# Optimization experiments

Hardware: AMD Instinct MI355X
Metric: run time of the kernel (lower is better)

## Reference

```python
import jax, jax.numpy as jnp
import numpy as np
import math

DIM = 512
HEADS = 8
B = 16
P = 2048
REL_MAX = 64
REL_SIZE = 2 * REL_MAX + 1
RANK = 4
ALPHA = 16.0
QBITS = 4


def simq(w, bits=QBITS):
    # symmetric linear fake-quantization (matches simulate_quantization)
    qmin = -2 ** (bits - 1)
    qmax = 2 ** (bits - 1) - 1
    m = jnp.max(jnp.abs(w))
    scale = m / qmax
    q = jnp.clip(jnp.round(w / (scale + 1e-8)), qmin, qmax) * scale
    return jnp.where(m == 0, w, q)


def lora_lin(x, W, b, A, LB):
    # F.linear with quantized weight/bias + LoRA path
    out = x @ simq(W).T + simq(b)
    return out + (x @ A.T @ LB.T) * (ALPHA / RANK)


def setup_inputs() -> dict:
    key = jax.random.key(0)
    ks = jax.random.split(key, 20)
    d2 = DIM * 2
    inp = {
        "curr_pos": 2048,
        "z_curr_ri": jax.random.normal(ks[0], (B, DIM, 2), jnp.float32),
        "z_past_ri": jax.random.normal(ks[1], (P, B, DIM, 2), jnp.float32),
        "rel_bias_ri": jax.random.normal(ks[2], (REL_SIZE, DIM, 2), jnp.float32) * 0.02,
    }
    names = ["q", "k", "v", "o"]
    for i, n in enumerate(names):
        kw, ka, kb = jax.random.split(ks[3 + i], 3)
        inp["W" + n] = jax.random.normal(kw, (d2, d2), jnp.float32) / math.sqrt(d2)
        inp["b" + n] = jnp.zeros((d2,), jnp.float32)
        inp["A" + n] = jax.random.normal(ka, (RANK, d2), jnp.float32) / math.sqrt(d2)
        inp["LB" + n] = jax.random.normal(kb, (d2, RANK), jnp.float32) * 0.01
    return inp


def reference(curr_pos, z_curr_ri, z_past_ri, rel_bias_ri,
              Wq, bq, Aq, LBq, Wk, bk, Ak, LBk,
              Wv, bv, Av, LBv, Wo, bo, Ao, LBo):
    Bsz = z_curr_ri.shape[0]
    past_len = z_past_ri.shape[0]
    dim = z_curr_ri.shape[1]
    hd = dim // HEADS

    # projections on real-view of complex inputs ([.., dim, 2] -> [.., 2*dim])
    q = lora_lin(z_curr_ri.reshape(Bsz, dim * 2), Wq, bq, Aq, LBq)
    k = lora_lin(z_past_ri.reshape(past_len, Bsz, dim * 2), Wk, bk, Ak, LBk)
    v = lora_lin(z_past_ri.reshape(past_len, Bsz, dim * 2), Wv, bv, Av, LBv)

    q = q.reshape(Bsz, HEADS, hd, 2)            # [B,H,hd,2]
    k = k.reshape(past_len, Bsz, HEADS, hd, 2)  # [P,B,H,hd,2]
    v = v.reshape(past_len, Bsz, HEADS, hd, 2)
    qr, qi = q[..., 0], q[..., 1]
    kr, ki = k[..., 0], k[..., 1]
    vr, vi = v[..., 0], v[..., 1]

    # Re(q * conj(k)) summed over head_dim -> [B,H,P]
    dot = jnp.einsum('bhd,pbhd->bhp', qr, kr) + jnp.einsum('bhd,pbhd->bhp', qi, ki)

    # relative positional bias lookup (clamped index)
    rel_d = jnp.arange(curr_pos - past_len, curr_pos)
    idx = jnp.clip(rel_d + REL_MAX, 0, rel_bias_ri.shape[0] - 1)
    rb = rel_bias_ri[idx].reshape(past_len, HEADS, hd, 2)  # [P,H,hd,2]
    rel = jnp.einsum('bhd,phd->bhp', qr, rb[..., 0]) + jnp.einsum('bhd,phd->bhp', qi, rb[..., 1])

    w = jax.nn.softmax((dot + rel) / math.sqrt(hd), axis=-1)  # [B,H,P]

    # real softmax weights applied to complex values
    out_r = jnp.einsum('bhp,pbhd->bhd', w, vr)
    out_i = jnp.einsum('bhp,pbhd->bhd', w, vi)
    out_ri = jnp.stack([out_r, out_i], axis=-1).reshape(Bsz, dim * 2)

    o = lora_lin(out_ri, Wo, bo, Ao, LBo)
    return o.reshape(Bsz, dim, 2)  # real view of complex output [B,dim]
```

## Files before the change

### kernel.cpp

```cpp
#include <hip/hip_runtime.h>
#include <math.h>

typedef _Float16 f16;
typedef _Float16 f16x8 __attribute__((ext_vector_type(8)));
typedef _Float16 f16x4 __attribute__((ext_vector_type(4)));
typedef float f32x4 __attribute__((ext_vector_type(4)));

#define NP 2048
#define M_ROWS 32768

#define OFF_ABSMAX 0u
#define OFF_TQ     256u
#define OFF_TO     512u
#define OFF_QBIAS  1024u
#define OFF_XQH    32768u
#define OFF_XQL    65536u
#define OFF_XOH    98304u
#define OFF_XOL    131072u
#define OFF_QBUF   163840u
#define OFF_ATT    229376u
#define OFF_PM     294912u
#define OFF_PL     299008u
#define OFF_PO     303104u
#define OFF_WH     1048576u
#define OFF_TK     9437184u
#define OFF_TV     9961472u
#define OFF_KV     10485760u

__device__ __forceinline__ float qint_of(float w, float scale) {
    return fminf(7.f, fmaxf(-8.f, rintf(w / (scale + 1e-8f))));
}

__device__ __forceinline__ void gload16(const void* g, void* l) {
  __builtin_amdgcn_global_load_lds((const __attribute__((address_space(1))) void*)g,
                                   (__attribute__((address_space(3))) void*)l, 16, 0, 0);
}

__global__ void __launch_bounds__(256) absmax_kernel(
    const float* __restrict__ W0, const float* __restrict__ W1,
    const float* __restrict__ W2, const float* __restrict__ W3,
    unsigned* __restrict__ absmax) {
  int mat = blockIdx.x >> 6;
  int blk = blockIdx.x & 63;
  const float* W = mat == 0 ? W0 : mat == 1 ? W1 : mat == 2 ? W2 : W3;
  int tid = blk * 256 + threadIdx.x;
  const float4* W4 = (const float4*)W;
  float m = 0.f;
  #pragma unroll
  for (int i = 0; i < 16; ++i) {
    float4 v = W4[tid + i * 16384];
    m = fmaxf(m, fmaxf(fmaxf(fabsf(v.x), fabsf(v.y)), fmaxf(fabsf(v.z), fabsf(v.w))));
  }
  #pragma unroll
  for (int k = 32; k >= 1; k >>= 1) m = fmaxf(m, __shfl_xor(m, k));
  __shared__ float sm[4];
  if ((threadIdx.x & 63) == 0) sm[threadIdx.x >> 6] = m;
  __syncthreads();
  if (threadIdx.x == 0) {
    m = fmaxf(fmaxf(sm[0], sm[1]), fmaxf(sm[2], sm[3]));
    atomicMax(&absmax[mat], __float_as_uint(m));
  }
}

__global__ void __launch_bounds__(256) bias_quant_kernel(
    const float* __restrict__ b0, const float* __restrict__ b1,
    const float* __restrict__ b2, const float* __restrict__ b3,
    float* __restrict__ qbias) {
  int mat = blockIdx.x;
  const float* bb = mat == 0 ? b0 : mat == 1 ? b1 : mat == 2 ? b2 : b3;
  int t = threadIdx.x;
  float4 v = ((const float4*)bb)[t];
  float m = fmaxf(fmaxf(fabsf(v.x), fabsf(v.y)), fmaxf(fabsf(v.z), fabsf(v.w)));
  #pragma unroll
  for (int k = 32; k >= 1; k >>= 1) m = fmaxf(m, __shfl_xor(m, k));
  __shared__ float sm[4];
  if ((t & 63) == 0) sm[t >> 6] = m;
  __syncthreads();
  float M = fmaxf(fmaxf(sm[0], sm[1]), fmaxf(sm[2], sm[3]));
  float scale = M * (1.0f / 7.0f);
  float4 q;
  q.x = (M == 0.f) ? v.x : qint_of(v.x, scale) * scale;
  q.y = (M == 0.f) ? v.y : qint_of(v.y, scale) * scale;
  q.z = (M == 0.f) ? v.z : qint_of(v.z, scale) * scale;
  q.w = (M == 0.f) ? v.w : qint_of(v.w, scale) * scale;
  ((float4*)(qbias + mat * 1024))[t] = q;
}

__global__ void __launch_bounds__(256) quantW_kernel(
    const float* __restrict__ W0, const float* __restrict__ W1,
    const float* __restrict__ W2, const float* __restrict__ W3,
    const unsigned* __restrict__ absmax, f16* __restrict__ Wh) {
  int gid = blockIdx.x * 256 + threadIdx.x;
  int mat = gid >> 18;
  int idx = gid & 262143;
  const float* W = mat == 0 ? W0 : mat == 1 ? W1 : mat == 2 ? W2 : W3;
  float scale = __uint_as_float(absmax[mat]) * (1.0f / 7.0f);
  float4 v = ((const float4*)W)[idx];
  f16x4 r;
  r[0] = (f16)qint_of(v.x, scale);
  r[1] = (f16)qint_of(v.y, scale);
  r[2] = (f16)qint_of(v.z, scale);
  r[3] = (f16)qint_of(v.w, scale);
  *(f16x4*)(Wh + (size_t)mat * 1048576 + (size_t)idx * 4) = r;
}

__global__ void __launch_bounds__(256) cvt_hilo_kernel(
    const float* __restrict__ x, f16* __restrict__ hi, f16* __restrict__ lo) {
  int i = blockIdx.x * 256 + threadIdx.x;
  float4 v = ((const float4*)x)[i];
  f16 h0 = (f16)v.x, h1 = (f16)v.y, h2 = (f16)v.z, h3 = (f16)v.w;
  f16x4 hv = {h0, h1, h2, h3};
  f16x4 lv = {(f16)(v.x - (float)h0), (f16)(v.y - (float)h1),
              (f16)(v.z - (float)h2), (f16)(v.w - (float)h3)};
  *(f16x4*)(hi + (size_t)i * 4) = hv;
  *(f16x4*)(lo + (size_t)i * 4) = lv;
}

__global__ void __launch_bounds__(256) lora_t_small_kernel(
    const float* __restrict__ x, const float* __restrict__ A, float* __restrict__ t) {
  int tt = threadIdx.x;
  int b = tt >> 4;
  int r = (tt >> 2) & 3;
  int s = tt & 3;
  const float4* xv = (const float4*)(x + b * 1024 + s * 256);
  const float4* av = (const float4*)(A + r * 1024 + s * 256);
  float acc = 0.f;
  #pragma unroll 4
  for (int i = 0; i < 64; ++i) {
    float4 a = xv[i], c = av[i];
    acc += a.x * c.x + a.y * c.y + a.z * c.z + a.w * c.w;
  }
  acc += __shfl_xor(acc, 1);
  acc += __shfl_xor(acc, 2);
  if (s == 0) t[b * 4 + r] = acc;
}

__global__ void __launch_bounds__(256) lora_t_big_kernel(
    const float* __restrict__ zp, const float* __restrict__ Ak,
    const float* __restrict__ Av, float* __restrict__ tk, float* __restrict__ tv,
    f16* __restrict__ zph, f16* __restrict__ zpl) {
  __shared__ float sA[8 * 1024];
  for (int i = 0; i < 8; ++i) {
    int f4 = threadIdx.x + i * 256;
    float4 v = (f4 < 1024) ? ((const float4*)Ak)[f4] : ((const float4*)Av)[f4 - 1024];
    ((float4*)sA)[f4] = v;
  }
  __syncthreads();
  int lane = threadIdx.x & 63, wave = threadIdx.x >> 6;
  for (int it = 0; it < 4; ++it) {
    int m = blockIdx.x * 16 + wave * 4 + it;
    const float4* xr = (const float4*)(zp + (size_t)m * 1024);
    float acc[8] = {0.f, 0.f, 0.f, 0.f, 0.f, 0.f, 0.f, 0.f};
    for (int c = lane; c < 256; c += 64) {
      float4 xv = xr[c];
      if (zph) {
        f16 h0 = (f16)xv.x, h1 = (f16)xv.y, h2 = (f16)xv.z, h3 = (f16)xv.w;
        f16x4 hv = {h0, h1, h2, h3};
        f16x4 lv = {(f16)(xv.x - (float)h0), (f16)(xv.y - (float)h1),
                    (f16)(xv.z - (float)h2), (f16)(xv.w - (float)h3)};
        *(f16x4*)(zph + (size_t)m * 1024 + c * 4) = hv;
        *(f16x4*)(zpl + (size_t)m * 1024 + c * 4) = lv;
      }
      #pragma unroll
      for (int r = 0; r < 8; ++r) {
        float4 a = ((const float4*)sA)[r * 256 + c];
        acc[r] += xv.x * a.x + xv.y * a.y + xv.z * a.z + xv.w * a.w;
      }
    }
    #pragma unroll
    for (int k = 32; k >= 1; k >>= 1) {
      #pragma unroll
      for (int r = 0; r < 8; ++r) acc[r] += __shfl_xor(acc[r], k);
    }
    if (lane == 0) {
      tk[m * 4 + 0] = acc[0]; tk[m * 4 + 1] = acc[1];
      tk[m * 4 + 2] = acc[2]; tk[m * 4 + 3] = acc[3];
      tv[m * 4 + 0] = acc[4]; tv[m * 4 + 1] = acc[5];
      tv[m * 4 + 2] = acc[6]; tv[m * 4 + 3] = acc[7];
    }
  }
}

__global__ void __launch_bounds__(256) gemv_mfma_kernel(
    const f16* __restrict__ xhi, const f16* __restrict__ xlo,
    const f16* __restrict__ Wm, const unsigned* __restrict__ absmax, int mat,
    const float* __restrict__ qb, const float* __restrict__ t,
    const float* __restrict__ LB, float* __restrict__ out) {
  int wave = threadIdx.x >> 6, lane = threadIdx.x & 63;
  int nf = blockIdx.x * 4 + wave;
  int n0 = nf * 16;
  int row = lane & 15, kq = lane >> 4;
  f32x4 acc = {0.f, 0.f, 0.f, 0.f};
  const f16* xh = xhi + row * 1024 + kq * 8;
  const f16* xl = xlo + row * 1024 + kq * 8;
  const f16* wp = Wm + (size_t)(n0 + row) * 1024 + kq * 8;
  #pragma unroll 4
  for (int k0 = 0; k0 < 1024; k0 += 32) {
    f16x8 ah = *(const f16x8*)(xh + k0);
    f16x8 al = *(const f16x8*)(xl + k0);
    f16x8 bb = *(const f16x8*)(wp + k0);
    acc = __builtin_amdgcn_mfma_f32_16x16x32_f16(ah, bb, acc, 0, 0, 0);
    acc = __builtin_amdgcn_mfma_f32_16x16x32_f16(al, bb, acc, 0, 0, 0);
  }
  float scale = __uint_as_float(absmax[mat]) * (1.0f / 7.0f);
  int col = n0 + row;
  float bias = qb[col];
  float4 lb = *(const float4*)(LB + col * 4);
  #pragma unroll
  for (int j = 0; j < 4; ++j) {
    int m = kq * 4 + j;
    float4 tvv = *(const float4*)(t + m * 4);
    out[m * 1024 + col] =
        scale * acc[j] + bias + 4.0f * (tvv.x * lb.x + tvv.y * lb.y + tvv.z * lb.z + tvv.w * lb.w);
  }
}

template <typename KVT>
__global__ void __launch_bounds__(256, 2) kv_gemm_kernel(
    const float* __restrict__ zp, const f16* __restrict__ Wh,
    const unsigned* __restrict__ absmax, const float* __restrict__ qbias,
    const float* __restrict__ tk, const float* __restrict__ tv,
    const float* __restrict__ LBk, const float* __restrict__ LBv,
    KVT* __restrict__ kout, KVT* __restrict__ vout) {
  __shared__ __align__(16) f16 sAh[128][40];
  __shared__ __align__(16) f16 sAl[128][40];
  __shared__ __align__(16) f16 sB[128][40];
  __shared__ float sT[128][4];

  int nb = blockIdx.x;
  int m0 = blockIdx.y * 128;
  bool is_v = nb >= 8;
  int n0 = (nb & 7) * 128;
  int mat = is_v ? 2 : 1;
  const f16* Wm = Wh + (size_t)mat * 1048576;
  const float* ttv = is_v ? tv : tk;
  const float* LBm = is_v ? LBv : LBk;
  const float* qb = qbias + mat * 1024;
  KVT* outp = is_v ? vout : kout;

  int tid = threadIdx.x;
  int lane = tid & 63, wave = tid >> 6;
  int wm = (wave >> 1) * 64, wn = (wave & 1) * 64;
  int row = lane & 15, kq = lane >> 4;

  f32x4 acc[4][4];
  #pragma unroll
  for (int i = 0; i < 4; ++i)
    #pragma unroll
    for (int j = 0; j < 4; ++j) acc[i][j] = (f32x4){0.f, 0.f, 0.f, 0.f};

  int sr = tid >> 1, seg = tid & 1;
  const float* asrc = zp + (size_t)(m0 + sr) * 1024 + seg * 16;
  const f16* bsrc = Wm + (size_t)(n0 + sr) * 1024 + seg * 16;

  for (int k0 = 0; k0 < 1024; k0 += 32) {
    __syncthreads();
    float xs[16];
    const float4* a4 = (const float4*)(asrc + k0);
    *(float4*)&xs[0] = a4[0];
    *(float4*)&xs[4] = a4[1];
    *(float4*)&xs[8] = a4[2];
    *(float4*)&xs[12] = a4[3];
    f16 hs[16], ls[16];
    #pragma unroll
    for (int i = 0; i < 16; ++i) {
      f16 h = (f16)xs[i];
      hs[i] = h;
      ls[i] = (f16)(xs[i] - (float)h);
    }
    *(f16x8*)&sAh[sr][seg * 16] = *(f16x8*)&hs[0];
    *(f16x8*)&sAh[sr][seg * 16 + 8] = *(f16x8*)&hs[8];
    *(f16x8*)&sAl[sr][seg * 16] = *(f16x8*)&ls[0];
    *(f16x8*)&sAl[sr][seg * 16 + 8] = *(f16x8*)&ls[8];
    const f16x8* b8 = (const f16x8*)(bsrc + k0);
    *(f16x8*)&sB[sr][seg * 16] = b8[0];
    *(f16x8*)&sB[sr][seg * 16 + 8] = b8[1];
    __syncthreads();
    f16x8 ah[4], al[4], bf[4];
    #pragma unroll
    for (int mi = 0; mi < 4; ++mi) {
      ah[mi] = *(const f16x8*)&sAh[wm + mi * 16 + row][kq * 8];
      al[mi] = *(const f16x8*)&sAl[wm + mi * 16 + row][kq * 8];
    }
    #pragma unroll
    for (int ni = 0; ni < 4; ++ni) bf[ni] = *(const f16x8*)&sB[wn + ni * 16 + row][kq * 8];
    #pragma unroll
    for (int mi = 0; mi < 4; ++mi)
      #pragma unroll
      for (int ni = 0; ni < 4; ++ni)
        acc[mi][ni] = __builtin_amdgcn_mfma_f32_16x16x32_f16(ah[mi], bf[ni], acc[mi][ni], 0, 0, 0);
    #pragma unroll
    for (int mi = 0; mi < 4; ++mi)
      #pragma unroll
      for (int ni = 0; ni < 4; ++ni)
        acc[mi][ni] = __builtin_amdgcn_mfma_f32_16x16x32_f16(al[mi], bf[ni], acc[mi][ni], 0, 0, 0);
  }
  ((float2*)sT)[tid] = ((const float2*)(ttv + (size_t)m0 * 4))[tid];
  __syncthreads();
  float scale = __uint_as_float(absmax[mat]) * (1.0f / 7.0f);
  #pragma unroll
  for (int ni = 0; ni < 4; ++ni) {
    int ncol = n0 + wn + ni * 16 + row;
    int h = ncol >> 7, d = ncol & 127;
    float4 lb = *(const float4*)(LBm + ncol * 4);
    float bias = qb[ncol];
    #pragma unroll
    for (int mi = 0; mi < 4; ++mi) {
      #pragma unroll
      for (int j = 0; j < 4; ++j) {
        int mloc = wm + mi * 16 + kq * 4 + j;
        int m = m0 + mloc;
        int p = m >> 4, b = m & 15;
        float4 t4 = *(const float4*)&sT[mloc][0];
        float val = scale * acc[mi][ni][j] + bias +
                    4.0f * (t4.x * lb.x + t4.y * lb.y + t4.z * lb.z + t4.w * lb.w);
        outp[(((size_t)(b * 8 + h)) * 2048 + p) * 128 + d] = (KVT)val;
      }
    }
  }
}

template <typename KVT>
__global__ void __launch_bounds__(256, 3) kv_gemm_fast_kernel(
    const f16* __restrict__ zph, const f16* __restrict__ zpl,
    const f16* __restrict__ Wh, const unsigned* __restrict__ absmax,
    const float* __restrict__ qbias, const float* __restrict__ tk,
    const float* __restrict__ tv, const float* __restrict__ LBk,
    const float* __restrict__ LBv, KVT* __restrict__ kout, KVT* __restrict__ vout) {
  __shared__ __align__(16) f16 sAh[8192];
  __shared__ __align__(16) f16 sAl[8192];
  __shared__ __align__(16) f16 sB[8192];
  __shared__ float sT[128][4];

  int nb = blockIdx.x;
  int m0 = blockIdx.y * 128;
  bool is_v = nb >= 8;
  int n0 = (nb & 7) * 128;
  int mat = is_v ? 2 : 1;
  const f16* Wm = Wh + (size_t)mat * 1048576;
  const float* ttv = is_v ? tv : tk;
  const float* LBm = is_v ? LBv : LBk;
  const float* qb = qbias + mat * 1024;
  KVT* outp = is_v ? vout : kout;

  int tid = threadIdx.x;
  int lane = tid & 63, wave = tid >> 6;
  int wm = (wave >> 1) * 64, wn = (wave & 1) * 64;
  int row = lane & 15, kq = lane >> 4;

  const f16* srcAh = zph + (size_t)m0 * 1024;
  const f16* srcAl = zpl + (size_t)m0 * 1024;
  const f16* srcB = Wm + (size_t)n0 * 1024;

  int goff[4], lbase[4];
  #pragma unroll
  for (int r = 0; r < 4; ++r) {
    int L = r * 256 + tid;
    int rw = L >> 3, cc = L & 7, cs = cc ^ (rw & 7);
    goff[r] = rw * 1024 + cs * 8;
    lbase[r] = (r * 256 + (wave << 6)) * 8;
  }

  f32x4 acc[4][4];
  #pragma unroll
  for (int i = 0; i < 4; ++i)
    #pragma unroll
    for (int j = 0; j < 4; ++j) acc[i][j] = (f32x4){0.f, 0.f, 0.f, 0.f};

  for (int k0 = 0; k0 < 1024; k0 += 64) {
    __syncthreads();
    #pragma unroll
    for (int r = 0; r < 4; ++r) {
      gload16(srcAh + goff[r] + k0, sAh + lbase[r]);
      gload16(srcAl + goff[r] + k0, sAl + lbase[r]);
      gload16(srcB + goff[r] + k0, sB + lbase[r]);
    }
    __syncthreads();
    #pragma unroll
    for (int ks = 0; ks < 2; ++ks) {
      int ch = (ks * 4 + kq) ^ (row & 7);
      f16x8 ah[4], al[4], bf[4];
      #pragma unroll
      for (int mi = 0; mi < 4; ++mi) {
        int ad = (wm + mi * 16 + row) * 64 + ch * 8;
        ah[mi] = *(const f16x8*)&sAh[ad];
        al[mi] = *(const f16x8*)&sAl[ad];
      }
      #pragma unroll
      for (int ni = 0; ni < 4; ++ni)
        bf[ni] = *(const f16x8*)&sB[(wn + ni * 16 + row) * 64 + ch * 8];
      #pragma unroll
      for (int mi = 0; mi < 4; ++mi)
        #pragma unroll
        for (int ni = 0; ni < 4; ++ni)
          acc[mi][ni] = __builtin_amdgcn_mfma_f32_16x16x32_f16(ah[mi], bf[ni], acc[mi][ni], 0, 0, 0);
      #pragma unroll
      for (int mi = 0; mi < 4; ++mi)
        #pragma unroll
        for (int ni = 0; ni < 4; ++ni)
          acc[mi][ni] = __builtin_amdgcn_mfma_f32_16x16x32_f16(al[mi], bf[ni], acc[mi][ni], 0, 0, 0);
    }
  }
  ((float2*)sT)[tid] = ((const float2*)(ttv + (size_t)m0 * 4))[tid];
  __syncthreads();
  float scale = __uint_as_float(absmax[mat]) * (1.0f / 7.0f);
  #pragma unroll
  for (int ni = 0; ni < 4; ++ni) {
    int ncol = n0 + wn + ni * 16 + row;
    int h = ncol >> 7, d = ncol & 127;
    float4 lb = *(const float4*)(LBm + ncol * 4);
    float bias = qb[ncol];
    #pragma unroll
    for (int mi = 0; mi < 4; ++mi) {
      #pragma unroll
      for (int j = 0; j < 4; ++j) {
        int mloc = wm + mi * 16 + kq * 4 + j;
        int m = m0 + mloc;
        int p = m >> 4, b = m & 15;
        float4 t4 = *(const float4*)&sT[mloc][0];
        float val = scale * acc[mi][ni][j] + bias +
                    4.0f * (t4.x * lb.x + t4.y * lb.y + t4.z * lb.z + t4.w * lb.w);
        outp[(((size_t)(b * 8 + h)) * 2048 + p) * 128 + d] = (KVT)val;
      }
    }
  }
}

template <typename KVT>
__device__ __forceinline__ float4 ld4(const KVT* p) {
  if constexpr (sizeof(KVT) == 4) {
    return *reinterpret_cast<const float4*>(p);
  } else {
    f16x4 v = *reinterpret_cast<const f16x4*>(p);
    return make_float4((float)v[0], (float)v[1], (float)v[2], (float)v[3]);
  }
}

template <typename KVT>
__global__ void __launch_bounds__(256) attn_part_kernel(
    const float* __restrict__ qbuf, const KVT* __restrict__ kbuf,
    const KVT* __restrict__ vbuf, const float* __restrict__ rel_bias,
    const int* __restrict__ curr_pos_p, float* __restrict__ m_part,
    float* __restrict__ l_part, float* __restrict__ o_part) {
  __shared__ float sS[256];
  __shared__ float red[8];
  __shared__ float sO[2][128];
  int bh = blockIdx.x;
  int c = blockIdx.y;
  int b = bh >> 3, h = bh & 7;
  int p0 = c * 256;
  int tid = threadIdx.x, lane = tid & 63, wave = tid >> 6;
  int j4 = lane & 31, ph = lane >> 5;
  float4 qv = *(const float4*)(qbuf + b * 1024 + h * 128 + j4 * 4);
  int off = *curr_pos_p - NP + 64;
  const KVT* kb = kbuf + ((size_t)bh * 2048 + p0) * 128;
  for (int i = 0; i < 32; ++i) {
    int pl = i * 8 + wave * 2 + ph;
    float4 kv = ld4(kb + (size_t)pl * 128 + j4 * 4);
    int idx = min(max(p0 + pl + off, 0), 128);
    float4 rb = *(const float4*)(rel_bias + idx * 1024 + h * 128 + j4 * 4);
    float a = qv.x * (kv.x + rb.x) + qv.y * (kv.y + rb.y) +
              qv.z * (kv.z + rb.z) + qv.w * (kv.w + rb.w);
    a += __shfl_xor(a, 16);
    a += __shfl_xor(a, 8);
    a += __shfl_xor(a, 4);
    a += __shfl_xor(a, 2);
    a += __shfl_xor(a, 1);
    if (j4 == 0) sS[pl] = a * 0.125f;
  }
  __syncthreads();
  float v = sS[tid];
  float mx = v;
  #pragma unroll
  for (int k = 32; k >= 1; k >>= 1) mx = fmaxf(mx, __shfl_xor(mx, k));
  if (lane == 0) red[wave] = mx;
  __syncthreads();
  mx = fmaxf(fmaxf(red[0], red[1]), fmaxf(red[2], red[3]));
  float e = expf(v - mx);
  sS[tid] = e;
  float sum = e;
  #pragma unroll
  for (int k = 32; k >= 1; k >>= 1) sum += __shfl_xor(sum, k);
  if (lane == 0) red[4 + wave] = sum;
  __syncthreads();
  float l = red[4] + red[5] + red[6] + red[7];
  int d = tid & 127, s = tid >> 7;
  const KVT* vb = vbuf + ((size_t)bh * 2048 + p0 + s * 128) * 128 + d;
  float acc = 0.f;
  #pragma unroll 4
  for (int i = 0; i < 128; ++i) acc += sS[s * 128 + i] * (float)vb[(size_t)i * 128];
  sO[s][d] = acc;
  __syncthreads();
  if (s == 0) {
    int pc = bh * 8 + c;
    o_part[pc * 128 + d] = sO[0][d] + sO[1][d];
    if (d == 0) {
      m_part[pc] = mx;
      l_part[pc] = l;
    }
  }
}

__global__ void __launch_bounds__(128) attn_combine_kernel(
    const float* __restrict__ m_part, const float* __restrict__ l_part,
    const float* __restrict__ o_part, float* __restrict__ attout) {
  int bh = blockIdx.x;
  int d = threadIdx.x;
  float M = -1e30f;
  #pragma unroll
  for (int c = 0; c < 8; ++c) M = fmaxf(M, m_part[bh * 8 + c]);
  float L = 0.f, o = 0.f;
  #pragma unroll
  for (int c = 0; c < 8; ++c) {
    float w = expf(m_part[bh * 8 + c] - M);
    L += w * l_part[bh * 8 + c];
    o += w * o_part[(bh * 8 + c) * 128 + d];
  }
  int b = bh >> 3, h = bh & 7;
  attout[b * 1024 + h * 128 + d] = o / L;
}

extern "C" void kernel_launch(void* const* d_in, const int* in_sizes, int n_in,
                              void* d_out, int out_size, void* d_ws, size_t ws_size,
                              hipStream_t stream) {
  const int* curr_pos = (const int*)d_in[0];
  const float* z_curr = (const float*)d_in[1];
  const float* z_past = (const float*)d_in[2];
  const float* rel_bias = (const float*)d_in[3];
  const float* Wq = (const float*)d_in[4];
  const float* bq = (const float*)d_in[5];
  const float* Aq = (const float*)d_in[6];
  const float* LBq = (const float*)d_in[7];
  const float* Wk = (const float*)d_in[8];
  const float* bk = (const float*)d_in[9];
  const float* Ak = (const float*)d_in[10];
  const float* LBk = (const float*)d_in[11];
  const float* Wv = (const float*)d_in[12];
  const float* bv = (const float*)d_in[13];
  const float* Av = (const float*)d_in[14];
  const float* LBv = (const float*)d_in[15];
  const float* Wo = (const float*)d_in[16];
  const float* bo = (const float*)d_in[17];
  const float* Ao = (const float*)d_in[18];
  const float* LBo = (const float*)d_in[19];

  char* ws = (char*)d_ws;
  unsigned* absmax = (unsigned*)(ws + OFF_ABSMAX);
  float* t_q = (float*)(ws + OFF_TQ);
  float* t_o = (float*)(ws + OFF_TO);
  float* qbias = (float*)(ws + OFF_QBIAS);
  f16* xqh = (f16*)(ws + OFF_XQH);
  f16* xql = (f16*)(ws + OFF_XQL);
  f16* xoh = (f16*)(ws + OFF_XOH);
  f16* xol = (f16*)(ws + OFF_XOL);
  float* qbuf = (float*)(ws + OFF_QBUF);
  float* attout = (float*)(ws + OFF_ATT);
  float* pm = (float*)(ws + OFF_PM);
  float* pl = (float*)(ws + OFF_PL);
  float* po = (float*)(ws + OFF_PO);
  f16* Wh = (f16*)(ws + OFF_WH);
  float* t_k = (float*)(ws + OFF_TK);
  float* t_v = (float*)(ws + OFF_TV);
  char* kvbase = ws + OFF_KV;

  bool f32kv = ws_size >= (size_t)OFF_KV + 2ull * 134217728ull;
  size_t kvBytes1 = f32kv ? 134217728ull : 67108864ull;
  f16* zph = (f16*)(kvbase + 2 * kvBytes1);
  f16* zpl = (f16*)(kvbase + 2 * kvBytes1 + 67108864ull);
  bool fast = ws_size >= (size_t)OFF_KV + 2 * kvBytes1 + 2ull * 67108864ull;

  hipMemsetAsync(absmax, 0, 16, stream);
  absmax_kernel<<<256, 256, 0, stream>>>(Wq, Wk, Wv, Wo, absmax);
  bias_quant_kernel<<<4, 256, 0, stream>>>(bq, bk, bv, bo, qbias);
  quantW_kernel<<<4096, 256, 0, stream>>>(Wq, Wk, Wv, Wo, absmax, Wh);
  cvt_hilo_kernel<<<16, 256, 0, stream>>>(z_curr, xqh, xql);
  lora_t_small_kernel<<<1, 256, 0, stream>>>(z_curr, Aq, t_q);
  gemv_mfma_kernel<<<16, 256, 0, stream>>>(xqh, xql, Wh, absmax, 0, qbias, t_q, LBq, qbuf);
  lora_t_big_kernel<<<2048, 256, 0, stream>>>(z_past, Ak, Av, t_k, t_v,
                                              fast ? zph : nullptr, fast ? zpl : nullptr);
  if (f32kv) {
    float* kb = (float*)kvbase;
    float* vb = (float*)(kvbase + kvBytes1);
    if (fast)
      kv_gemm_fast_kernel<float><<<dim3(16, 256), 256, 0, stream>>>(
          zph, zpl, Wh, absmax, qbias, t_k, t_v, LBk, LBv, kb, vb);
    else
      kv_gemm_kernel<float><<<dim3(16, 256), 256, 0, stream>>>(
          z_past, Wh, absmax, qbias, t_k, t_v, LBk, LBv, kb, vb);
    attn_part_kernel<float><<<dim3(128, 8), 256, 0, stream>>>(
        qbuf, kb, vb, rel_bias, curr_pos, pm, pl, po);
  } else {
    f16* kb = (f16*)kvbase;
    f16* vb = (f16*)(kvbase + kvBytes1);
    if (fast)
      kv_gemm_fast_kernel<f16><<<dim3(16, 256), 256, 0, stream>>>(
          zph, zpl, Wh, absmax, qbias, t_k, t_v, LBk, LBv, kb, vb);
    else
      kv_gemm_kernel<f16><<<dim3(16, 256), 256, 0, stream>>>(
          z_past, Wh, absmax, qbias, t_k, t_v, LBk, LBv, kb, vb);
    attn_part_kernel<f16><<<dim3(128, 8), 256, 0, stream>>>(
        qbuf, kb, vb, rel_bias, curr_pos, pm, pl, po);
  }
  attn_combine_kernel<<<128, 128, 0, stream>>>(pm, pl, po, attout);
  cvt_hilo_kernel<<<16, 256, 0, stream>>>(attout, xoh, xol);
  lora_t_small_kernel<<<1, 256, 0, stream>>>(attout, Ao, t_o);
  gemv_mfma_kernel<<<16, 256, 0, stream>>>(xoh, xol, Wh + 3ull * 1048576ull, absmax, 3,
                                           qbias + 3 * 1024, t_o, LBo, (float*)d_out);
}
```

Before: 875.4 us.

## Stage KV GEMM epilogue through LDS, swizzle blocks per XCD, vectorize PV loop

The KV projection kernel now writes its epilogue tile into LDS (reusing the operand buffers) in two halves, then stores full 128-wide rows with vector writes instead of scattered scalar stores. Block indices are remapped so that consecutive M tiles are grouped per XCD, which should improve L2 reuse of the A rows. The attention partial kernel's P·V loop now uses float4 vector loads over 8 position groups, with a reduction through shared memory. This adds extra barriers and LDS traffic in the epilogue.

After: 827.1 us. 5.5% less time.

```diff
diff --git a/kernel.cpp b/kernel.cpp
--- a/kernel.cpp
+++ b/kernel.cpp
@@ -327,16 +327,24 @@
     const float* __restrict__ qbias, const float* __restrict__ tk,
     const float* __restrict__ tv, const float* __restrict__ LBk,
     const float* __restrict__ LBv, KVT* __restrict__ kout, KVT* __restrict__ vout) {
-  __shared__ __align__(16) f16 sAh[8192];
-  __shared__ __align__(16) f16 sAl[8192];
-  __shared__ __align__(16) f16 sB[8192];
+  __shared__ __align__(16) f16 sbuf[24576];
   __shared__ float sT[128][4];
-
-  int nb = blockIdx.x;
-  int m0 = blockIdx.y * 128;
+  f16* sAh = sbuf;
+  f16* sAl = sbuf + 8192;
+  f16* sB = sbuf + 16384;
+  float* tbuf = (float*)sbuf;
+
+  int linear = blockIdx.x + (blockIdx.y << 4);
+  int xcd = linear & 7;
+  int slot = linear >> 3;
+  int nb = slot & 15;
+  int g = ((slot >> 4) << 3) + xcd;
+  int m0 = g << 7;
+
   bool is_v = nb >= 8;
   int n0 = (nb & 7) * 128;
   int mat = is_v ? 2 : 1;
+  int h = nb & 7;
   const f16* Wm = Wh + (size_t)mat * 1048576;
   const float* ttv = is_v ? tv : tk;
   const float* LBm = is_v ? LBv : LBk;
@@ -404,23 +412,48 @@
   ((float2*)sT)[tid] = ((const float2*)(ttv + (size_t)m0 * 4))[tid];
   __syncthreads();
   float scale = __uint_as_float(absmax[mat]) * (1.0f / 7.0f);
+  float biasv[4];
+  float4 lbv[4];
   #pragma unroll
   for (int ni = 0; ni < 4; ++ni) {
     int ncol = n0 + wn + ni * 16 + row;
-    int h = ncol >> 7, d = ncol & 127;
-    float4 lb = *(const float4*)(LBm + ncol * 4);
-    float bias = qb[ncol];
-    #pragma unroll
-    for (int mi = 0; mi < 4; ++mi) {
-      #pragma unroll
-      for (int j = 0; j < 4; ++j) {
-        int mloc = wm + mi * 16 + kq * 4 + j;
-        int m = m0 + mloc;
-        int p = m >> 4, b = m & 15;
-        float4 t4 = *(const float4*)&sT[mloc][0];
-        float val = scale * acc[mi][ni][j] + bias +
-                    4.0f * (t4.x * lb.x + t4.y * lb.y + t4.z * lb.z + t4.w * lb.w);
-        outp[(((size_t)(b * 8 + h)) * 2048 + p) * 128 + d] = (KVT)val;
+    biasv[ni] = qb[ncol];
+    lbv[ni] = *(const float4*)(LBm + ncol * 4);
+  }
+  int lh = lane >> 5, l5 = lane & 31;
+  #pragma unroll
+  for (int halfsel = 0; halfsel < 2; ++halfsel) {
+    __syncthreads();
+    if ((wave >> 1) == halfsel) {
+      #pragma unroll
+      for (int ni = 0; ni < 4; ++ni) {
+        #pragma unroll
+        for (int mi = 0; mi < 4; ++mi) {
+          #pragma unroll
+          for (int j = 0; j < 4; ++j) {
+            int ml = mi * 16 + kq * 4 + j;
+            float4 t4 = *(const float4*)&sT[wm + ml][0];
+            tbuf[ml * 132 + wn + ni * 16 + row] =
+                scale * acc[mi][ni][j] + biasv[ni] +
+                4.0f * (t4.x * lbv[ni].x + t4.y * lbv[ni].y + t4.z * lbv[ni].z +
+                        t4.w * lbv[ni].w);
+          }
+        }
+      }
+    }
+    __syncthreads();
+    #pragma unroll
+    for (int it = 0; it < 8; ++it) {
+      int ml = it * 8 + wave * 2 + lh;
+      int m = m0 + halfsel * 64 + ml;
+      int p = m >> 4, b = m & 15;
+      float4 v = *(const float4*)&tbuf[ml * 132 + l5 * 4];
+      KVT* dst = outp + (((size_t)(b * 8 + h)) * 2048 + p) * 128 + l5 * 4;
+      if constexpr (sizeof(KVT) == 4) {
+        *(float4*)dst = v;
+      } else {
+        f16x4 hv = {(f16)v.x, (f16)v.y, (f16)v.z, (f16)v.w};
+        *(f16x4*)dst = hv;
       }
     }
   }
@@ -444,7 +477,7 @@
     float* __restrict__ l_part, float* __restrict__ o_part) {
   __shared__ float sS[256];
   __shared__ float red[8];
-  __shared__ float sO[2][128];
+  __shared__ float sOv[8][132];
   int bh = blockIdx.x;
   int c = blockIdx.y;
   int b = bh >> 3, h = bh & 7;
@@ -484,17 +517,27 @@
   if (lane == 0) red[4 + wave] = sum;
   __syncthreads();
   float l = red[4] + red[5] + red[6] + red[7];
-  int d = tid & 127, s = tid >> 7;
-  const KVT* vb = vbuf + ((size_t)bh * 2048 + p0 + s * 128) * 128 + d;
-  float acc = 0.f;
+  int d4 = tid & 31, pg = tid >> 5;
+  const KVT* vb = vbuf + ((size_t)bh * 2048 + p0 + pg * 32) * 128;
+  float4 a4 = make_float4(0.f, 0.f, 0.f, 0.f);
   #pragma unroll 4
-  for (int i = 0; i < 128; ++i) acc += sS[s * 128 + i] * (float)vb[(size_t)i * 128];
-  sO[s][d] = acc;
-  __syncthreads();
-  if (s == 0) {
+  for (int i = 0; i < 32; ++i) {
+    float s = sS[pg * 32 + i];
+    float4 vv = ld4(vb + (size_t)i * 128 + d4 * 4);
+    a4.x += s * vv.x;
+    a4.y += s * vv.y;
+    a4.z += s * vv.z;
+    a4.w += s * vv.w;
+  }
+  *(float4*)&sOv[pg][d4 * 4] = a4;
+  __syncthreads();
+  if (tid < 128) {
+    float o = 0.f;
+    #pragma unroll
+    for (int gI = 0; gI < 8; ++gI) o += sOv[gI][tid];
     int pc = bh * 8 + c;
-    o_part[pc * 128 + d] = sO[0][d] + sO[1][d];
-    if (d == 0) {
+    o_part[pc * 128 + tid] = o;
+    if (tid == 0) {
       m_part[pc] = mx;
       l_part[pc] = l;
     }
```
